# Kernel optimization log

Measured on AMD Instinct MI355X. Metric: run time of the kernel, lower is better.

Reference implementation:

```python
import jax, jax.numpy as jnp
import numpy as np

B = 2
NCLS = 19    # semantic classes for the logits heads
NLAB = 20    # raw point label values 0..19 (0 = unlabeled)
# (Z, Y, X) grids at strides 2, 4, 8 of sizes=[256,256,32]
GRIDS = {2: (16, 128, 128), 4: (8, 64, 64), 8: (4, 32, 32)}


def _lin_idx(coord, Z, Y, X):
    # coord: (N,4) int rows [b, z, y, x] -> flat cell index over B*Z*Y*X
    b, z, y, x = coord[:, 0], coord[:, 1], coord[:, 2], coord[:, 3]
    return ((b * Z + z) * Y + y) * X + x


def _bev_projection(feat, coord, Y, X):
    # Fused equivalent of torch.unique + scatter_max + spconv dense():
    # scatter_max features directly into the dense (B, Y, X) BEV grid keyed by (b,y,x).
    key = (coord[:, 0] * Y + coord[:, 2]) * X + coord[:, 3]
    C = feat.shape[1]
    dense = jax.ops.segment_max(feat, key, num_segments=B * Y * X)  # empty cells -> -inf
    dense = jnp.where(jnp.isfinite(dense), dense, jnp.zeros((), feat.dtype))
    return dense.reshape(B, Y, X, C).transpose(0, 3, 1, 2)  # (B, C, Y, X)


def _voxel_sem_target(fcoord, pcoord, plabel, Z, Y, X):
    # Majority-vote semantic label per point voxel, gathered at feature voxel coords.
    ncell = B * Z * Y * X
    pair = _lin_idx(pcoord, Z, Y, X) * NLAB + plabel  # (cell, label) key
    counts = jax.ops.segment_sum(
        jnp.ones(pcoord.shape[0], jnp.int32), pair, num_segments=ncell * NLAB
    ).reshape(ncell, NLAB)
    maj = jnp.argmax(counts, axis=1).astype(jnp.int32)   # most frequent label per cell
    occ = counts.sum(axis=1) > 0                          # cell contains any point
    fk = _lin_idx(fcoord, Z, Y, X)
    return jnp.where(occ[fk], maj[fk], 0).astype(jnp.int32)  # unmatched -> 0


def _head(x, w1, g, b, w2, b2):
    # Linear(no bias) -> BatchNorm1d(train stats) -> LeakyReLU(0.1) -> Linear
    h = x @ w1
    mu = h.mean(axis=0)
    var = h.var(axis=0)
    h = (h - mu) * jax.lax.rsqrt(var + 1e-5) * g + b
    h = jnp.where(h >= 0, h, 0.1 * h)
    return h @ w2 + b2


def _rand_coords(key, n, Z, Y, X):
    kb, kz, ky, kx = jax.random.split(key, 4)
    return jnp.stack([
        jax.random.randint(kb, (n,), 0, B, dtype=jnp.int32),
        jax.random.randint(kz, (n,), 0, Z, dtype=jnp.int32),
        jax.random.randint(ky, (n,), 0, Y, dtype=jnp.int32),
        jax.random.randint(kx, (n,), 0, X, dtype=jnp.int32),
    ], axis=1)


def setup_inputs() -> dict:
    key = jax.random.key(0)
    ks = jax.random.split(key, 32)
    M1, M2, M3, NP = 200000, 100000, 50000, 500000
    inp = {
        'proj1_vw': jax.random.normal(ks[0], (M1, 64), jnp.float32),
        'proj2_vw': jax.random.normal(ks[1], (M2, 128), jnp.float32),
        'proj3_vw': jax.random.normal(ks[2], (M3, 256), jnp.float32),
        'vw1_coord': _rand_coords(ks[3], M1, *GRIDS[2]),
        'vw2_coord': _rand_coords(ks[4], M2, *GRIDS[4]),
        'vw3_coord': _rand_coords(ks[5], M3, *GRIDS[8]),
        'idx02': _rand_coords(ks[6], NP, *GRIDS[2]),
        'idx04': _rand_coords(ks[7], NP, *GRIDS[4]),
        'idx08': _rand_coords(ks[8], NP, *GRIDS[8]),
        'pw_label': jax.random.randint(ks[9], (NP,), 0, NLAB, dtype=jnp.int32),
    }
    # learned head parameters (out2 / out4 / out8)
    def head_params(k, cin):
        k1, k2 = jax.random.split(k)
        return (jax.random.normal(k1, (cin, 64), jnp.float32) * 0.02,
                jnp.ones((64,), jnp.float32), jnp.zeros((64,), jnp.float32),
                jax.random.normal(k2, (64, NCLS), jnp.float32) * 0.02,
                jnp.zeros((NCLS,), jnp.float32))
    for tag, k, cin in (('h2', ks[10], 64), ('h4', ks[11], 128), ('h8', ks[12], 256)):
        w1, g, b, w2, b2 = head_params(k, cin)
        inp[f'{tag}_w1'], inp[f'{tag}_g'], inp[f'{tag}_b'] = w1, g, b
        inp[f'{tag}_w2'], inp[f'{tag}_b2'] = w2, b2
    return inp


def reference(proj1_vw, proj2_vw, proj3_vw, vw1_coord, vw2_coord, vw3_coord,
              idx02, idx04, idx08, pw_label,
              h2_w1, h2_g, h2_b, h2_w2, h2_b2,
              h4_w1, h4_g, h4_b, h4_w2, h4_b2,
              h8_w1, h8_g, h8_b, h8_w2, h8_b2):
    (Z2, Y2, X2), (Z4, Y4, X4), (Z8, Y8, X8) = GRIDS[2], GRIDS[4], GRIDS[8]
    bev1 = _bev_projection(proj1_vw, vw1_coord, Y2, X2)   # (B, 64, 128, 128)
    bev2 = _bev_projection(proj2_vw, vw2_coord, Y4, X4)   # (B, 128, 64, 64)
    bev3 = _bev_projection(proj3_vw, vw3_coord, Y8, X8)   # (B, 256, 32, 32)
    lbl2 = _voxel_sem_target(vw1_coord, idx02, pw_label, Z2, Y2, X2)
    lbl4 = _voxel_sem_target(vw2_coord, idx04, pw_label, Z4, Y4, X4)
    lbl8 = _voxel_sem_target(vw3_coord, idx08, pw_label, Z8, Y8, X8)
    log2 = _head(proj1_vw, h2_w1, h2_g, h2_b, h2_w2, h2_b2)
    log4 = _head(proj2_vw, h4_w1, h4_g, h4_b, h4_w2, h4_b2)
    log8 = _head(proj3_vw, h8_w1, h8_g, h8_b, h8_w2, h8_b2)
    return (bev1, bev2, bev3, log2, log4, log8, lbl2, lbl4, lbl8)
```

## Files before the change

### kernel.cpp

```cpp
#include <hip/hip_runtime.h>
#include <hip/hip_bf16.h>

typedef unsigned int u32;
typedef unsigned short u16;
typedef __attribute__((ext_vector_type(8))) short short8;
typedef __attribute__((ext_vector_type(4))) float f32x4;

#define NLAB 20

#define M_1 200000
#define C_1 64
#define Z_1 16
#define Y_1 128
#define X_1 128

#define M_2 100000
#define C_2 128
#define Z_2 8
#define Y_2 64
#define X_2 64

#define M_3 50000
#define C_3 256
#define Z_3 4
#define Y_3 32
#define X_3 32

#define O_BEV1 0
#define O_BEV2 2097152
#define O_BEV3 3145728
#define O_LOG1 3670016
#define O_LOG2 7470016
#define O_LOG3 9370016
#define O_LBL1 10320016
#define O_LBL2 10520016
#define O_LBL3 10620016

#define WB_CNT 0
#define WB_CUR 43008
#define WB_PIDX 86016
#define NCELLS 43008
#define SB1 0
#define SB2 32768
#define SB3 40960

#define WBEV_F  4194304
#define WBEV2_F 6291456
#define WBEV3_F 7340032

#define WC1_W 8388608
#define WC2_W 11010048
#define WC3_W 11337728
#define W_COUNT_BYTES 11960320ull
#define WH1 0
#define WH2 12800000
#define WH3 19200000
#define WPART 12000000
#define WP1 0
#define WP2 200064
#define WP3 300160
#define WSTATS 12350208

#define GB1 1563
#define GB2 782
#define GB3 391
#define HB1 782
#define HB2 391
#define HB3 196

static __device__ __forceinline__ u16 f2bf(float f) {
  u32 u = __float_as_uint(f);
  u32 r = u + 0x7fffu + ((u >> 16) & 1u);
  return (u16)(r >> 16);
}

__global__ __launch_bounds__(256) void k_cc(
    const int* __restrict__ co1, const int* __restrict__ co2, const int* __restrict__ co3,
    int* __restrict__ cnt,
    const int* __restrict__ i2, const int* __restrict__ i4, const int* __restrict__ i8,
    const int* __restrict__ lab, u32* __restrict__ hist)
{
  int blk = blockIdx.x;
  if (blk < HB1 + HB2 + HB3) {
    const int* co; int Y, X, M, base, m;
    if (blk < HB1)            { co = co1; Y = Y_1; X = X_1; M = M_1; base = SB1; m = blk * 256 + threadIdx.x; }
    else if (blk < HB1 + HB2) { co = co2; Y = Y_2; X = X_2; M = M_2; base = SB2; m = (blk - HB1) * 256 + threadIdx.x; }
    else                      { co = co3; Y = Y_3; X = X_3; M = M_3; base = SB3; m = (blk - HB1 - HB2) * 256 + threadIdx.x; }
    if (m >= M) return;
    int4 c = *(const int4*)(co + m * 4);
    atomicAdd(cnt + base + (c.x * Y + c.z) * X + c.w, 1);
  } else {
    int cb = blk - (HB1 + HB2 + HB3);
    const int* pc; int Z, Y, X; u32* base; int i;
    if (cb < 1954)      { pc = i2; Z = Z_1; Y = Y_1; X = X_1; base = hist + WC1_W; i = cb * 256 + threadIdx.x; }
    else if (cb < 3908) { pc = i4; Z = Z_2; Y = Y_2; X = X_2; base = hist + WC2_W; i = (cb - 1954) * 256 + threadIdx.x; }
    else                { pc = i8; Z = Z_3; Y = Y_3; X = X_3; base = hist + WC3_W; i = (cb - 3908) * 256 + threadIdx.x; }
    if (i >= 500000) return;
    int4 c = *(const int4*)(pc + i * 4);
    int l = lab[i];
    int lin = ((c.x * Z + c.y) * Y + c.z) * X + c.w;
    atomicAdd(base + lin * 5 + (l >> 2), 1u << ((l & 3) * 8));
  }
}

__global__ __launch_bounds__(1024) void k_scan(const int* __restrict__ cnt, int* __restrict__ cur) {
  int t = threadIdx.x;
  int local[42];
  int s = 0;
#pragma unroll
  for (int j = 0; j < 42; j++) { local[j] = cnt[t * 42 + j]; s += local[j]; }
  __shared__ int red[1024];
  red[t] = s;
  __syncthreads();
  for (int off = 1; off < 1024; off <<= 1) {
    int v = (t >= off) ? red[t - off] : 0;
    __syncthreads();
    red[t] += v;
    __syncthreads();
  }
  int base = red[t] - s;
#pragma unroll
  for (int j = 0; j < 42; j++) { cur[t * 42 + j] = base; base += local[j]; }
}

__global__ __launch_bounds__(256) void k_scatter(
    const int* __restrict__ co1, const int* __restrict__ co2, const int* __restrict__ co3,
    int* __restrict__ cur, int* __restrict__ pidx)
{
  int blk = blockIdx.x;
  const int* co; int Y, X, M, base, m;
  if (blk < HB1)            { co = co1; Y = Y_1; X = X_1; M = M_1; base = SB1; m = blk * 256 + threadIdx.x; }
  else if (blk < HB1 + HB2) { co = co2; Y = Y_2; X = X_2; M = M_2; base = SB2; m = (blk - HB1) * 256 + threadIdx.x; }
  else                      { co = co3; Y = Y_3; X = X_3; M = M_3; base = SB3; m = (blk - HB1 - HB2) * 256 + threadIdx.x; }
  if (m >= M) return;
  int4 c = *(const int4*)(co + m * 4);
  int slot = atomicAdd(cur + base + (c.x * Y + c.z) * X + c.w, 1);
  pidx[slot] = m;
}

#define GBATCH 8
__global__ __launch_bounds__(256) void k_bevgather(
    const float* __restrict__ f1, const float* __restrict__ f2, const float* __restrict__ f3,
    const int* __restrict__ cnt, const int* __restrict__ cur,
    const int* __restrict__ pidx, float* __restrict__ ws)
{
  int w = blockIdx.x * 4 + (threadIdx.x >> 6);
  int lane = threadIdx.x & 63;
  int t0 = w * 4;
  int C = (t0 < 32768) ? 64 : (t0 < 49152) ? 128 : 256;
  const float* fp[4]; int n[4], end_[4]; u32 wb[4];
#pragma unroll
  for (int k = 0; k < 4; k++) {
    int t = t0 + k; const float* f; int cidx; u32 wbv;
    if (t < 32768) {
      f = f1; cidx = SB1 + t; wbv = WBEV_F + (u32)t * 64;
    } else if (t < 49152) {
      int u = t - 32768; int cell = u >> 1, ch = (u & 1) * 64;
      f = f2 + ch; cidx = SB2 + cell; wbv = WBEV2_F + (u32)cell * 128 + ch;
    } else {
      int u = t - 49152; int cell = u >> 2, ch = (u & 3) * 64;
      f = f3 + ch; cidx = SB3 + cell; wbv = WBEV3_F + (u32)cell * 256 + ch;
    }
    fp[k] = f; n[k] = cnt[cidx]; end_[k] = cur[cidx]; wb[k] = wbv;
  }
  int maxn = max(max(n[0], n[1]), max(n[2], n[3]));
  float acc[4];
#pragma unroll
  for (int k = 0; k < 4; k++) acc[k] = __uint_as_float(0xff800000u);
  for (int base = 0; base < maxn; base += GBATCH) {
    int p[4][GBATCH];
#pragma unroll
    for (int k = 0; k < 4; k++) {
      int s = end_[k] - n[k] + base;
      int hi = end_[k] - 1;
#pragma unroll
      for (int j = 0; j < GBATCH; j++) {
        int idx = s + j;
        idx = idx < hi ? idx : hi;
        idx = idx > 0 ? idx : 0;
        p[k][j] = pidx[idx];
      }
    }
    float v[4][GBATCH];
#pragma unroll
    for (int k = 0; k < 4; k++)
#pragma unroll
      for (int j = 0; j < GBATCH; j++)
        v[k][j] = fp[k][(size_t)p[k][j] * C + lane];
#pragma unroll
    for (int k = 0; k < 4; k++)
#pragma unroll
      for (int j = 0; j < GBATCH; j++)
        acc[k] = fmaxf(acc[k], v[k][j]);
  }
#pragma unroll
  for (int k = 0; k < 4; k++)
    ws[wb[k] + lane] = (n[k] > 0) ? acc[k] : 0.f;
}

__global__ __launch_bounds__(256) void k_tl(
    const float* __restrict__ ws, const u32* __restrict__ hist,
    const int* __restrict__ fc1, const int* __restrict__ fc2, const int* __restrict__ fc3,
    float* __restrict__ out)
{
  int blk = blockIdx.x;
  int tid = threadIdx.x;
  if (blk < HB1 + HB2 + HB3) {
    const int* fc; int Z, Y, X, M; const u32* base; long lbase; int m;
    if (blk < HB1)            { fc = fc1; Z = Z_1; Y = Y_1; X = X_1; M = M_1; base = hist + WC1_W; lbase = O_LBL1; m = blk * 256 + tid; }
    else if (blk < HB1 + HB2) { fc = fc2; Z = Z_2; Y = Y_2; X = X_2; M = M_2; base = hist + WC2_W; lbase = O_LBL2; m = (blk - HB1) * 256 + tid; }
    else                      { fc = fc3; Z = Z_3; Y = Y_3; X = X_3; M = M_3; base = hist + WC3_W; lbase = O_LBL3; m = (blk - HB1 - HB2) * 256 + tid; }
    if (m >= M) return;
    int4 c = *(const int4*)(fc + m * 4);
    int lin = ((c.x * Z + c.y) * Y + c.z) * X + c.w;
    const u32* cp = base + lin * 5;
    u32 w0 = cp[0], w1 = cp[1], w2 = cp[2], w3 = cp[3], w4 = cp[4];
    int best = (int)(w0 & 0xffu); int bi = 0;
#pragma unroll
    for (int n = 1; n < NLAB; n++) {
      u32 w = (n < 4) ? w0 : (n < 8) ? w1 : (n < 12) ? w2 : (n < 16) ? w3 : w4;
      int cc = (int)((w >> ((n & 3) * 8)) & 0xffu);
      if (cc > best) { best = cc; bi = n; }
    }
    out[lbase + m] = (float)bi;
    return;
  }
  __shared__ float tileU[4160];
  int bid = blk - (HB1 + HB2 + HB3);
  if (bid < 512) {
    int b = bid >> 8, y = (bid >> 1) & 127, x0 = (bid & 1) * 64;
    const float* src = ws + WBEV_F + (size_t)((b * 128 + y) * 128 + x0) * 64;
#pragma unroll
    for (int pass = 0; pass < 16; pass++) {
      int idx = pass * 256 + tid;
      int x = idx >> 6, c = idx & 63;
      tileU[x * 65 + c] = src[(size_t)x * 64 + c];
    }
    __syncthreads();
    size_t ob = O_BEV1 + ((size_t)(b * 64) * 128 + y) * 128 + x0;
#pragma unroll
    for (int pass = 0; pass < 16; pass++) {
      int idx = pass * 256 + tid;
      int c = idx >> 6, x = idx & 63;
      out[ob + (size_t)c * 16384 + x] = tileU[x * 65 + c];
    }
  } else if (bid < 768) {
    int t = bid - 512;
    int b = t >> 7, y = (t >> 1) & 63, x0 = (t & 1) * 32;
    const float* src = ws + WBEV2_F + (size_t)((b * 64 + y) * 64 + x0) * 128;
#pragma unroll
    for (int pass = 0; pass < 16; pass++) {
      int idx = pass * 256 + tid;
      int x = idx >> 7, c = idx & 127;
      tileU[x * 129 + c] = src[(size_t)x * 128 + c];
    }
    __syncthreads();
    size_t ob = O_BEV2 + ((size_t)(b * 128) * 64 + y) * 64 + x0;
#pragma unroll
    for (int pass = 0; pass < 16; pass++) {
      int idx = pass * 256 + tid;
      int c = idx >> 5, x = idx & 31;
      out[ob + (size_t)c * 4096 + x] = tileU[x * 129 + c];
    }
  } else {
    int t = bid - 768;
    int b = t >> 6, y = (t >> 1) & 31, ch0 = (t & 1) * 128;
    const float* src = ws + WBEV3_F + (size_t)((b * 32 + y) * 32) * 256 + ch0;
#pragma unroll
    for (int pass = 0; pass < 16; pass++) {
      int idx = pass * 256 + tid;
      int x = idx >> 7, c = idx & 127;
      tileU[x * 129 + c] = src[(size_t)x * 256 + c];
    }
    __syncthreads();
    size_t ob = O_BEV3 + ((size_t)(b * 256 + ch0) * 32 + y) * 32;
#pragma unroll
    for (int pass = 0; pass < 16; pass++) {
      int idx = pass * 256 + tid;
      int c = idx >> 5, x = idx & 31;
      out[ob + (size_t)c * 1024 + x] = tileU[x * 129 + c];
    }
  }
}

__global__ __launch_bounds__(256) void k_gemm(
    const float* __restrict__ x1, const float* __restrict__ x2, const float* __restrict__ x3,
    const float* __restrict__ w1a, const float* __restrict__ w1b, const float* __restrict__ w1c,
    u16* __restrict__ hbuf, float* __restrict__ part)
{
  int blk = blockIdx.x;
  const float* x; const float* w1; u16* h; float* pp; int Cin, M, bl, NB;
  if (blk < GB1)            { x = x1; w1 = w1a; h = hbuf + WH1; pp = part + WP1; Cin = C_1; M = M_1; bl = blk;             NB = GB1; }
  else if (blk < GB1 + GB2) { x = x2; w1 = w1b; h = hbuf + WH2; pp = part + WP2; Cin = C_2; M = M_2; bl = blk - GB1;       NB = GB2; }
  else                      { x = x3; w1 = w1c; h = hbuf + WH3; pp = part + WP3; Cin = C_3; M = M_3; bl = blk - GB1 - GB2; NB = GB3; }
  int tid = threadIdx.x;
  int lane = tid & 63, wv = tid >> 6;
  int m16 = lane & 15, quad = lane >> 4;

  __shared__ u16 As[128 * 72];
  __shared__ u16 Bs[64 * 72];
  __shared__ float redS[4][64];
  __shared__ float redQ[4][64];

  f32x4 acc[2][4];
#pragma unroll
  for (int mt = 0; mt < 2; mt++)
#pragma unroll
    for (int nt = 0; nt < 4; nt++) acc[mt][nt] = (f32x4){0.f, 0.f, 0.f, 0.f};

  int nchunk = Cin >> 6;
  for (int c = 0; c < nchunk; c++) {
    if (c) __syncthreads();
#pragma unroll
    for (int pass = 0; pass < 8; pass++) {
      int fidx = pass * 256 + tid;
      int row = fidx >> 4, kp = (fidx & 15) * 4;
      int grow = bl * 128 + row;
      float4 v = make_float4(0.f, 0.f, 0.f, 0.f);
      if (grow < M) v = *(const float4*)(x + (size_t)grow * Cin + c * 64 + kp);
      ushort4 o = { f2bf(v.x), f2bf(v.y), f2bf(v.z), f2bf(v.w) };
      *(ushort4*)(As + row * 72 + kp) = o;
    }
    {
      int n = tid & 63, kg = tid >> 6;
#pragma unroll
      for (int p = 0; p < 4; p++) {
        int k0 = kg * 4 + p * 16;
        const float* wp = w1 + (size_t)(c * 64 + k0) * 64 + n;
        ushort4 o = { f2bf(wp[0]), f2bf(wp[64]), f2bf(wp[128]), f2bf(wp[192]) };
        *(ushort4*)(Bs + n * 72 + k0) = o;
      }
    }
    __syncthreads();
#pragma unroll
    for (int ks = 0; ks < 2; ks++) {
      short8 a0 = *(const short8*)(As + (wv * 32 + m16) * 72 + ks * 32 + quad * 8);
      short8 a1 = *(const short8*)(As + (wv * 32 + 16 + m16) * 72 + ks * 32 + quad * 8);
      short8 b[4];
#pragma unroll
      for (int nt = 0; nt < 4; nt++)
        b[nt] = *(const short8*)(Bs + (nt * 16 + m16) * 72 + ks * 32 + quad * 8);
#pragma unroll
      for (int nt = 0; nt < 4; nt++) {
        acc[0][nt] = __builtin_amdgcn_mfma_f32_16x16x32_bf16(a0, b[nt], acc[0][nt], 0, 0, 0);
        acc[1][nt] = __builtin_amdgcn_mfma_f32_16x16x32_bf16(a1, b[nt], acc[1][nt], 0, 0, 0);
      }
    }
  }

  float s[4] = {0.f, 0.f, 0.f, 0.f}, q[4] = {0.f, 0.f, 0.f, 0.f};
#pragma unroll
  for (int mt = 0; mt < 2; mt++) {
#pragma unroll
    for (int nt = 0; nt < 4; nt++) {
#pragma unroll
      for (int r = 0; r < 4; r++) {
        float v = acc[mt][nt][r];
        int grow = bl * 128 + wv * 32 + mt * 16 + quad * 4 + r;
        if (grow < M) h[(size_t)grow * 64 + nt * 16 + m16] = f2bf(v);
        s[nt] += v;
        q[nt] = fmaf(v, v, q[nt]);
      }
    }
  }
#pragma unroll
  for (int nt = 0; nt < 4; nt++) {
    s[nt] += __shfl_xor(s[nt], 16); s[nt] += __shfl_xor(s[nt], 32);
    q[nt] += __shfl_xor(q[nt], 16); q[nt] += __shfl_xor(q[nt], 32);
  }
  if (lane < 16) {
#pragma unroll
    for (int nt = 0; nt < 4; nt++) {
      redS[wv][nt * 16 + lane] = s[nt];
      redQ[wv][nt * 16 + lane] = q[nt];
    }
  }
  __syncthreads();
  if (tid < 64) {
    pp[tid * NB + bl] = redS[0][tid] + redS[1][tid] + redS[2][tid] + redS[3][tid];
  } else if (tid < 128) {
    int n2 = tid - 64;
    pp[(64 + n2) * NB + bl] = redQ[0][n2] + redQ[1][n2] + redQ[2][n2] + redQ[3][n2];
  }
}

__global__ __launch_bounds__(256) void k_stats(const float* __restrict__ part, float* __restrict__ stats,
    const float* __restrict__ g1, const float* __restrict__ b1,
    const float* __restrict__ g4, const float* __restrict__ b4,
    const float* __restrict__ g8, const float* __restrict__ b8)
{
  int blk = blockIdx.x;
  int sc = blk >> 6, col = blk & 63;
  int nb; const float* p; float invM; const float* g; const float* bb;
  if (sc == 0)      { nb = GB1; p = part + WP1; invM = 1.f / M_1; g = g1; bb = b1; }
  else if (sc == 1) { nb = GB2; p = part + WP2; invM = 1.f / M_2; g = g4; bb = b4; }
  else              { nb = GB3; p = part + WP3; invM = 1.f / M_3; g = g8; bb = b8; }
  int t = threadIdx.x;
  const float* ps = p + (size_t)col * nb;
  const float* pq = p + (size_t)(64 + col) * nb;
  float s = 0.f, q = 0.f;
  for (int i = t; i < nb; i += 256) { s += ps[i]; q += pq[i]; }
  __shared__ float r1[256], r2[256];
  r1[t] = s; r2[t] = q;
  __syncthreads();
  for (int off = 128; off > 0; off >>= 1) {
    if (t < off) { r1[t] += r1[t + off]; r2[t] += r2[t + off]; }
    __syncthreads();
  }
  if (t == 0) {
    float mu  = r1[0] * invM;
    float var = r2[0] * invM - mu * mu;
    float scale = rsqrtf(var + 1e-5f) * g[col];
    stats[sc * 128 + col]      = scale;
    stats[sc * 128 + 64 + col] = fmaf(-mu, scale, bb[col]);
  }
}

__global__ __launch_bounds__(256) void k_head(
    const u16* __restrict__ hbuf, const float* __restrict__ stats,
    const float* __restrict__ w21, const float* __restrict__ c21,
    const float* __restrict__ w24, const float* __restrict__ c24,
    const float* __restrict__ w28, const float* __restrict__ c28,
    float* __restrict__ out)
{
  int blk = blockIdx.x;
  const u16* h; const float* st; const float* w2; const float* b2;
  int M; long obase; int bl;
  if (blk < HB1)            { h = hbuf + WH1; st = stats;       w2 = w21; b2 = c21; M = M_1; obase = O_LOG1; bl = blk; }
  else if (blk < HB1 + HB2) { h = hbuf + WH2; st = stats + 128; w2 = w24; b2 = c24; M = M_2; obase = O_LOG2; bl = blk - HB1; }
  else                      { h = hbuf + WH3; st = stats + 256; w2 = w28; b2 = c28; M = M_3; obase = O_LOG3; bl = blk - HB1 - HB2; }
  int tid = threadIdx.x;
  int rowbase = bl * 256;
  int avail = M - rowbase; if (avail > 256) avail = 256;

  __shared__ __align__(16) float os[256 * 19];

  float acc[19];
#pragma unroll
  for (int n = 0; n < 19; n++) acc[n] = 0.f;

  if (tid < avail) {
    const uint4* hr = (const uint4*)(h + (size_t)(rowbase + tid) * 64);
    uint4 d[8];
#pragma unroll
    for (int q = 0; q < 8; q++) d[q] = hr[q];
#pragma unroll
    for (int q = 0; q < 8; q++) {
#pragma unroll
      for (int half = 0; half < 2; half++) {
        u32 dx = half ? d[q].z : d[q].x;
        u32 dy = half ? d[q].w : d[q].y;
        int j = q * 8 + half * 4;
        float f0 = __uint_as_float(dx << 16);
        float f1 = __uint_as_float(dx & 0xffff0000u);
        float f2 = __uint_as_float(dy << 16);
        float f3 = __uint_as_float(dy & 0xffff0000u);
        float a0 = fmaf(f0, st[j],     st[64 + j]);     a0 = a0 >= 0.f ? a0 : 0.1f * a0;
        float a1 = fmaf(f1, st[j + 1], st[64 + j + 1]); a1 = a1 >= 0.f ? a1 : 0.1f * a1;
        float a2 = fmaf(f2, st[j + 2], st[64 + j + 2]); a2 = a2 >= 0.f ? a2 : 0.1f * a2;
        float a3 = fmaf(f3, st[j + 3], st[64 + j + 3]); a3 = a3 >= 0.f ? a3 : 0.1f * a3;
#pragma unroll
        for (int n = 0; n < 19; n++) {
          acc[n] = fmaf(a0, w2[j * 19 + n], acc[n]);
          acc[n] = fmaf(a1, w2[(j + 1) * 19 + n], acc[n]);
          acc[n] = fmaf(a2, w2[(j + 2) * 19 + n], acc[n]);
          acc[n] = fmaf(a3, w2[(j + 3) * 19 + n], acc[n]);
        }
      }
    }
#pragma unroll
    for (int n = 0; n < 19; n++) os[tid * 19 + n] = acc[n] + b2[n];
  }
  __syncthreads();
  int tot = avail * 19;
  float* op = out + obase + (size_t)rowbase * 19;
  for (int i = tid; i < tot; i += 256) op[i] = os[i];
}

extern "C" void kernel_launch(void* const* d_in, const int* in_sizes, int n_in,
                              void* d_out, int out_size, void* d_ws, size_t ws_size,
                              hipStream_t stream) {
  (void)in_sizes; (void)n_in; (void)out_size; (void)ws_size;
  const float* p1 = (const float*)d_in[0];
  const float* p2 = (const float*)d_in[1];
  const float* p3 = (const float*)d_in[2];
  const int* vc1  = (const int*)d_in[3];
  const int* vc2  = (const int*)d_in[4];
  const int* vc3  = (const int*)d_in[5];
  const int* i2   = (const int*)d_in[6];
  const int* i4   = (const int*)d_in[7];
  const int* i8   = (const int*)d_in[8];
  const int* lab  = (const int*)d_in[9];
  const float* h2w1 = (const float*)d_in[10]; const float* h2g = (const float*)d_in[11];
  const float* h2b  = (const float*)d_in[12]; const float* h2w2 = (const float*)d_in[13];
  const float* h2b2 = (const float*)d_in[14];
  const float* h4w1 = (const float*)d_in[15]; const float* h4g = (const float*)d_in[16];
  const float* h4b  = (const float*)d_in[17]; const float* h4w2 = (const float*)d_in[18];
  const float* h4b2 = (const float*)d_in[19];
  const float* h8w1 = (const float*)d_in[20]; const float* h8g = (const float*)d_in[21];
  const float* h8b  = (const float*)d_in[22]; const float* h8w2 = (const float*)d_in[23];
  const float* h8b2 = (const float*)d_in[24];

  float* out = (float*)d_out;
  int* wsi = (int*)d_ws;
  u32* wsu = (u32*)d_ws;
  float* wsf = (float*)d_ws;
  u16* wsh = (u16*)d_ws;

  hipMemsetAsync(wsi + WB_CNT, 0, NCELLS * sizeof(int), stream);
  hipMemsetAsync(wsu + WC1_W, 0, W_COUNT_BYTES, stream);

  k_cc<<<HB1 + HB2 + HB3 + 5862, 256, 0, stream>>>(vc1, vc2, vc3, wsi + WB_CNT,
      i2, i4, i8, lab, wsu);
  k_scan<<<1, 1024, 0, stream>>>(wsi + WB_CNT, wsi + WB_CUR);
  k_scatter<<<HB1 + HB2 + HB3, 256, 0, stream>>>(vc1, vc2, vc3, wsi + WB_CUR, wsi + WB_PIDX);

  k_bevgather<<<3584, 256, 0, stream>>>(p1, p2, p3,
      wsi + WB_CNT, wsi + WB_CUR, wsi + WB_PIDX, wsf);

  k_tl<<<HB1 + HB2 + HB3 + 896, 256, 0, stream>>>(wsf, wsu, vc1, vc2, vc3, out);

  k_gemm<<<GB1 + GB2 + GB3, 256, 0, stream>>>(p1, p2, p3, h2w1, h4w1, h8w1, wsh, wsf + WPART);
  k_stats<<<192, 256, 0, stream>>>(wsf + WPART, wsf + WSTATS, h2g, h2b, h4g, h4b, h8g, h8b);
  k_head<<<HB1 + HB2 + HB3, 256, 0, stream>>>((const u16*)d_ws, wsf + WSTATS,
      h2w2, h2b2, h4w2, h4b2, h8w2, h8b2, out);
}
```

Before: 464.2 us.

## Fuse GEMM, BEV gather and label histogram into one mega-kernel launch

When the workspace is large enough, the pipeline is rescheduled. Only the cell count runs first, then one kernel runs the head GEMM, the BEV gather and the label histogram together. The BN stats reduction is folded into the label/transpose kernel, and the GEMM outputs move to non-overlapping workspace regions so they can run alongside the gather. This removes launches and lets independent, differently bounded work share the GPU, at the cost of more workspace and a larger heterogeneous grid. A fallback keeps the old sequence when the workspace is small.

```diff
diff --git a/kernel.cpp b/kernel.cpp
--- a/kernel.cpp
+++ b/kernel.cpp
@@ -52,14 +52,20 @@
 #define WC2_W 11010048
 #define WC3_W 11337728
 #define W_COUNT_BYTES 11960320ull
+
 #define WH1 0
 #define WH2 12800000
 #define WH3 19200000
-#define WPART 12000000
 #define WP1 0
 #define WP2 200064
 #define WP3 300160
-#define WSTATS 12350208
+
+#define WPART_SMALL 12000000
+#define WSTATS_SMALL 12350208
+#define WH_BIG_U16  22806528
+#define WPART_BIG   22603264
+#define WSTATS_BIG  22953472
+#define WS_BIG_NEED 92000000ull
 
 #define GB1 1563
 #define GB2 782
@@ -74,78 +80,40 @@
   return (u16)(r >> 16);
 }
 
-__global__ __launch_bounds__(256) void k_cc(
-    const int* __restrict__ co1, const int* __restrict__ co2, const int* __restrict__ co3,
-    int* __restrict__ cnt,
-    const int* __restrict__ i2, const int* __restrict__ i4, const int* __restrict__ i8,
-    const int* __restrict__ lab, u32* __restrict__ hist)
-{
-  int blk = blockIdx.x;
-  if (blk < HB1 + HB2 + HB3) {
-    const int* co; int Y, X, M, base, m;
-    if (blk < HB1)            { co = co1; Y = Y_1; X = X_1; M = M_1; base = SB1; m = blk * 256 + threadIdx.x; }
-    else if (blk < HB1 + HB2) { co = co2; Y = Y_2; X = X_2; M = M_2; base = SB2; m = (blk - HB1) * 256 + threadIdx.x; }
-    else                      { co = co3; Y = Y_3; X = X_3; M = M_3; base = SB3; m = (blk - HB1 - HB2) * 256 + threadIdx.x; }
-    if (m >= M) return;
-    int4 c = *(const int4*)(co + m * 4);
-    atomicAdd(cnt + base + (c.x * Y + c.z) * X + c.w, 1);
-  } else {
-    int cb = blk - (HB1 + HB2 + HB3);
-    const int* pc; int Z, Y, X; u32* base; int i;
-    if (cb < 1954)      { pc = i2; Z = Z_1; Y = Y_1; X = X_1; base = hist + WC1_W; i = cb * 256 + threadIdx.x; }
-    else if (cb < 3908) { pc = i4; Z = Z_2; Y = Y_2; X = X_2; base = hist + WC2_W; i = (cb - 1954) * 256 + threadIdx.x; }
-    else                { pc = i8; Z = Z_3; Y = Y_3; X = X_3; base = hist + WC3_W; i = (cb - 3908) * 256 + threadIdx.x; }
-    if (i >= 500000) return;
-    int4 c = *(const int4*)(pc + i * 4);
-    int l = lab[i];
-    int lin = ((c.x * Z + c.y) * Y + c.z) * X + c.w;
-    atomicAdd(base + lin * 5 + (l >> 2), 1u << ((l & 3) * 8));
-  }
-}
-
-__global__ __launch_bounds__(1024) void k_scan(const int* __restrict__ cnt, int* __restrict__ cur) {
-  int t = threadIdx.x;
-  int local[42];
-  int s = 0;
-#pragma unroll
-  for (int j = 0; j < 42; j++) { local[j] = cnt[t * 42 + j]; s += local[j]; }
-  __shared__ int red[1024];
-  red[t] = s;
-  __syncthreads();
-  for (int off = 1; off < 1024; off <<= 1) {
-    int v = (t >= off) ? red[t - off] : 0;
-    __syncthreads();
-    red[t] += v;
-    __syncthreads();
-  }
-  int base = red[t] - s;
-#pragma unroll
-  for (int j = 0; j < 42; j++) { cur[t * 42 + j] = base; base += local[j]; }
-}
-
-__global__ __launch_bounds__(256) void k_scatter(
-    const int* __restrict__ co1, const int* __restrict__ co2, const int* __restrict__ co3,
-    int* __restrict__ cur, int* __restrict__ pidx)
-{
-  int blk = blockIdx.x;
+
+static __device__ __forceinline__ void dev_cellcount(int blk, int tid,
+    const int* co1, const int* co2, const int* co3, int* cnt)
+{
   const int* co; int Y, X, M, base, m;
-  if (blk < HB1)            { co = co1; Y = Y_1; X = X_1; M = M_1; base = SB1; m = blk * 256 + threadIdx.x; }
-  else if (blk < HB1 + HB2) { co = co2; Y = Y_2; X = X_2; M = M_2; base = SB2; m = (blk - HB1) * 256 + threadIdx.x; }
-  else                      { co = co3; Y = Y_3; X = X_3; M = M_3; base = SB3; m = (blk - HB1 - HB2) * 256 + threadIdx.x; }
+  if (blk < HB1)            { co = co1; Y = Y_1; X = X_1; M = M_1; base = SB1; m = blk * 256 + tid; }
+  else if (blk < HB1 + HB2) { co = co2; Y = Y_2; X = X_2; M = M_2; base = SB2; m = (blk - HB1) * 256 + tid; }
+  else                      { co = co3; Y = Y_3; X = X_3; M = M_3; base = SB3; m = (blk - HB1 - HB2) * 256 + tid; }
   if (m >= M) return;
   int4 c = *(const int4*)(co + m * 4);
-  int slot = atomicAdd(cur + base + (c.x * Y + c.z) * X + c.w, 1);
-  pidx[slot] = m;
+  atomicAdd(cnt + base + (c.x * Y + c.z) * X + c.w, 1);
+}
+
+static __device__ __forceinline__ void dev_count(int cb, int tid,
+    const int* i2, const int* i4, const int* i8, const int* lab, u32* hist)
+{
+  const int* pc; int Z, Y, X; u32* base; int i;
+  if (cb < 1954)      { pc = i2; Z = Z_1; Y = Y_1; X = X_1; base = hist + WC1_W; i = cb * 256 + tid; }
+  else if (cb < 3908) { pc = i4; Z = Z_2; Y = Y_2; X = X_2; base = hist + WC2_W; i = (cb - 1954) * 256 + tid; }
+  else                { pc = i8; Z = Z_3; Y = Y_3; X = X_3; base = hist + WC3_W; i = (cb - 3908) * 256 + tid; }
+  if (i >= 500000) return;
+  int4 c = *(const int4*)(pc + i * 4);
+  int l = lab[i];
+  int lin = ((c.x * Z + c.y) * Y + c.z) * X + c.w;
+  atomicAdd(base + lin * 5 + (l >> 2), 1u << ((l & 3) * 8));
 }
 
 #define GBATCH 8
-__global__ __launch_bounds__(256) void k_bevgather(
-    const float* __restrict__ f1, const float* __restrict__ f2, const float* __restrict__ f3,
-    const int* __restrict__ cnt, const int* __restrict__ cur,
-    const int* __restrict__ pidx, float* __restrict__ ws)
-{
-  int w = blockIdx.x * 4 + (threadIdx.x >> 6);
-  int lane = threadIdx.x & 63;
+static __device__ __forceinline__ void dev_gather(int gb, int tid,
+    const float* f1, const float* f2, const float* f3,
+    const int* cnt, const int* cur, const int* pidx, float* ws)
+{
+  int w = gb * 4 + (tid >> 6);
+  int lane = tid & 63;
   int t0 = w * 4;
   int C = (t0 < 32768) ? 64 : (t0 < 49152) ? 128 : 256;
   const float* fp[4]; int n[4], end_[4]; u32 wb[4];
@@ -198,102 +166,15 @@
     ws[wb[k] + lane] = (n[k] > 0) ? acc[k] : 0.f;
 }
 
-__global__ __launch_bounds__(256) void k_tl(
-    const float* __restrict__ ws, const u32* __restrict__ hist,
-    const int* __restrict__ fc1, const int* __restrict__ fc2, const int* __restrict__ fc3,
-    float* __restrict__ out)
-{
-  int blk = blockIdx.x;
-  int tid = threadIdx.x;
-  if (blk < HB1 + HB2 + HB3) {
-    const int* fc; int Z, Y, X, M; const u32* base; long lbase; int m;
-    if (blk < HB1)            { fc = fc1; Z = Z_1; Y = Y_1; X = X_1; M = M_1; base = hist + WC1_W; lbase = O_LBL1; m = blk * 256 + tid; }
-    else if (blk < HB1 + HB2) { fc = fc2; Z = Z_2; Y = Y_2; X = X_2; M = M_2; base = hist + WC2_W; lbase = O_LBL2; m = (blk - HB1) * 256 + tid; }
-    else                      { fc = fc3; Z = Z_3; Y = Y_3; X = X_3; M = M_3; base = hist + WC3_W; lbase = O_LBL3; m = (blk - HB1 - HB2) * 256 + tid; }
-    if (m >= M) return;
-    int4 c = *(const int4*)(fc + m * 4);
-    int lin = ((c.x * Z + c.y) * Y + c.z) * X + c.w;
-    const u32* cp = base + lin * 5;
-    u32 w0 = cp[0], w1 = cp[1], w2 = cp[2], w3 = cp[3], w4 = cp[4];
-    int best = (int)(w0 & 0xffu); int bi = 0;
-#pragma unroll
-    for (int n = 1; n < NLAB; n++) {
-      u32 w = (n < 4) ? w0 : (n < 8) ? w1 : (n < 12) ? w2 : (n < 16) ? w3 : w4;
-      int cc = (int)((w >> ((n & 3) * 8)) & 0xffu);
-      if (cc > best) { best = cc; bi = n; }
-    }
-    out[lbase + m] = (float)bi;
-    return;
-  }
-  __shared__ float tileU[4160];
-  int bid = blk - (HB1 + HB2 + HB3);
-  if (bid < 512) {
-    int b = bid >> 8, y = (bid >> 1) & 127, x0 = (bid & 1) * 64;
-    const float* src = ws + WBEV_F + (size_t)((b * 128 + y) * 128 + x0) * 64;
-#pragma unroll
-    for (int pass = 0; pass < 16; pass++) {
-      int idx = pass * 256 + tid;
-      int x = idx >> 6, c = idx & 63;
-      tileU[x * 65 + c] = src[(size_t)x * 64 + c];
-    }
-    __syncthreads();
-    size_t ob = O_BEV1 + ((size_t)(b * 64) * 128 + y) * 128 + x0;
-#pragma unroll
-    for (int pass = 0; pass < 16; pass++) {
-      int idx = pass * 256 + tid;
-      int c = idx >> 6, x = idx & 63;
-      out[ob + (size_t)c * 16384 + x] = tileU[x * 65 + c];
-    }
-  } else if (bid < 768) {
-    int t = bid - 512;
-    int b = t >> 7, y = (t >> 1) & 63, x0 = (t & 1) * 32;
-    const float* src = ws + WBEV2_F + (size_t)((b * 64 + y) * 64 + x0) * 128;
-#pragma unroll
-    for (int pass = 0; pass < 16; pass++) {
-      int idx = pass * 256 + tid;
-      int x = idx >> 7, c = idx & 127;
-      tileU[x * 129 + c] = src[(size_t)x * 128 + c];
-    }
-    __syncthreads();
-    size_t ob = O_BEV2 + ((size_t)(b * 128) * 64 + y) * 64 + x0;
-#pragma unroll
-    for (int pass = 0; pass < 16; pass++) {
-      int idx = pass * 256 + tid;
-      int c = idx >> 5, x = idx & 31;
-      out[ob + (size_t)c * 4096 + x] = tileU[x * 129 + c];
-    }
-  } else {
-    int t = bid - 768;
-    int b = t >> 6, y = (t >> 1) & 31, ch0 = (t & 1) * 128;
-    const float* src = ws + WBEV3_F + (size_t)((b * 32 + y) * 32) * 256 + ch0;
-#pragma unroll
-    for (int pass = 0; pass < 16; pass++) {
-      int idx = pass * 256 + tid;
-      int x = idx >> 7, c = idx & 127;
-      tileU[x * 129 + c] = src[(size_t)x * 256 + c];
-    }
-    __syncthreads();
-    size_t ob = O_BEV3 + ((size_t)(b * 256 + ch0) * 32 + y) * 32;
-#pragma unroll
-    for (int pass = 0; pass < 16; pass++) {
-      int idx = pass * 256 + tid;
-      int c = idx >> 5, x = idx & 31;
-      out[ob + (size_t)c * 1024 + x] = tileU[x * 129 + c];
-    }
-  }
-}
-
-__global__ __launch_bounds__(256) void k_gemm(
-    const float* __restrict__ x1, const float* __restrict__ x2, const float* __restrict__ x3,
-    const float* __restrict__ w1a, const float* __restrict__ w1b, const float* __restrict__ w1c,
-    u16* __restrict__ hbuf, float* __restrict__ part)
-{
-  int blk = blockIdx.x;
+static __device__ __forceinline__ void dev_gemm(int blk, int tid,
+    const float* x1, const float* x2, const float* x3,
+    const float* w1a, const float* w1b, const float* w1c,
+    u16* hbuf, float* part)
+{
   const float* x; const float* w1; u16* h; float* pp; int Cin, M, bl, NB;
   if (blk < GB1)            { x = x1; w1 = w1a; h = hbuf + WH1; pp = part + WP1; Cin = C_1; M = M_1; bl = blk;             NB = GB1; }
   else if (blk < GB1 + GB2) { x = x2; w1 = w1b; h = hbuf + WH2; pp = part + WP2; Cin = C_2; M = M_2; bl = blk - GB1;       NB = GB2; }
   else                      { x = x3; w1 = w1c; h = hbuf + WH3; pp = part + WP3; Cin = C_3; M = M_3; bl = blk - GB1 - GB2; NB = GB3; }
-  int tid = threadIdx.x;
   int lane = tid & 63, wv = tid >> 6;
   int m16 = lane & 15, quad = lane >> 4;
 
@@ -384,35 +265,231 @@
   }
 }
 
-__global__ __launch_bounds__(256) void k_stats(const float* __restrict__ part, float* __restrict__ stats,
-    const float* __restrict__ g1, const float* __restrict__ b1,
-    const float* __restrict__ g4, const float* __restrict__ b4,
-    const float* __restrict__ g8, const float* __restrict__ b8)
-{
-  int blk = blockIdx.x;
-  int sc = blk >> 6, col = blk & 63;
+static __device__ __forceinline__ void dev_lbl(int blk, int tid,
+    const int* fc1, const int* fc2, const int* fc3, const u32* hist, float* out)
+{
+  const int* fc; int Z, Y, X, M; const u32* base; long lbase; int m;
+  if (blk < HB1)            { fc = fc1; Z = Z_1; Y = Y_1; X = X_1; M = M_1; base = hist + WC1_W; lbase = O_LBL1; m = blk * 256 + tid; }
+  else if (blk < HB1 + HB2) { fc = fc2; Z = Z_2; Y = Y_2; X = X_2; M = M_2; base = hist + WC2_W; lbase = O_LBL2; m = (blk - HB1) * 256 + tid; }
+  else                      { fc = fc3; Z = Z_3; Y = Y_3; X = X_3; M = M_3; base = hist + WC3_W; lbase = O_LBL3; m = (blk - HB1 - HB2) * 256 + tid; }
+  if (m >= M) return;
+  int4 c = *(const int4*)(fc + m * 4);
+  int lin = ((c.x * Z + c.y) * Y + c.z) * X + c.w;
+  const u32* cp = base + lin * 5;
+  u32 w0 = cp[0], w1 = cp[1], w2 = cp[2], w3 = cp[3], w4 = cp[4];
+  int best = (int)(w0 & 0xffu); int bi = 0;
+#pragma unroll
+  for (int n = 1; n < NLAB; n++) {
+    u32 w = (n < 4) ? w0 : (n < 8) ? w1 : (n < 12) ? w2 : (n < 16) ? w3 : w4;
+    int cc = (int)((w >> ((n & 3) * 8)) & 0xffu);
+    if (cc > best) { best = cc; bi = n; }
+  }
+  out[lbase + m] = (float)bi;
+}
+
+static __device__ __forceinline__ void dev_transpose(int bid, int tid,
+    const float* ws, float* out)
+{
+  __shared__ float tileU[4160];
+  if (bid < 512) {
+    int b = bid >> 8, y = (bid >> 1) & 127, x0 = (bid & 1) * 64;
+    const float* src = ws + WBEV_F + (size_t)((b * 128 + y) * 128 + x0) * 64;
+#pragma unroll
+    for (int pass = 0; pass < 16; pass++) {
+      int idx = pass * 256 + tid;
+      int x = idx >> 6, c = idx & 63;
+      tileU[x * 65 + c] = src[(size_t)x * 64 + c];
+    }
+    __syncthreads();
+    size_t ob = O_BEV1 + ((size_t)(b * 64) * 128 + y) * 128 + x0;
+#pragma unroll
+    for (int pass = 0; pass < 16; pass++) {
+      int idx = pass * 256 + tid;
+      int c = idx >> 6, x = idx & 63;
+      out[ob + (size_t)c * 16384 + x] = tileU[x * 65 + c];
+    }
+  } else if (bid < 768) {
+    int t = bid - 512;
+    int b = t >> 7, y = (t >> 1) & 63, x0 = (t & 1) * 32;
+    const float* src = ws + WBEV2_F + (size_t)((b * 64 + y) * 64 + x0) * 128;
+#pragma unroll
+    for (int pass = 0; pass < 16; pass++) {
+      int idx = pass * 256 + tid;
+      int x = idx >> 7, c = idx & 127;
+      tileU[x * 129 + c] = src[(size_t)x * 128 + c];
+    }
+    __syncthreads();
+    size_t ob = O_BEV2 + ((size_t)(b * 128) * 64 + y) * 64 + x0;
+#pragma unroll
+    for (int pass = 0; pass < 16; pass++) {
+      int idx = pass * 256 + tid;
+      int c = idx >> 5, x = idx & 31;
+      out[ob + (size_t)c * 4096 + x] = tileU[x * 129 + c];
+    }
+  } else {
+    int t = bid - 768;
+    int b = t >> 6, y = (t >> 1) & 31, ch0 = (t & 1) * 128;
+    const float* src = ws + WBEV3_F + (size_t)((b * 32 + y) * 32) * 256 + ch0;
+#pragma unroll
+    for (int pass = 0; pass < 16; pass++) {
+      int idx = pass * 256 + tid;
+      int x = idx >> 7, c = idx & 127;
+      tileU[x * 129 + c] = src[(size_t)x * 256 + c];
+    }
+    __syncthreads();
+    size_t ob = O_BEV3 + ((size_t)(b * 256 + ch0) * 32 + y) * 32;
+#pragma unroll
+    for (int pass = 0; pass < 16; pass++) {
+      int idx = pass * 256 + tid;
+      int c = idx >> 5, x = idx & 31;
+      out[ob + (size_t)c * 1024 + x] = tileU[x * 129 + c];
+    }
+  }
+}
+
+static __device__ __forceinline__ void dev_stats(int sblk, int tid,
+    const float* part, float* stats,
+    const float* g1, const float* b1, const float* g4, const float* b4,
+    const float* g8, const float* b8)
+{
+  int sc = sblk >> 6, col = sblk & 63;
   int nb; const float* p; float invM; const float* g; const float* bb;
   if (sc == 0)      { nb = GB1; p = part + WP1; invM = 1.f / M_1; g = g1; bb = b1; }
   else if (sc == 1) { nb = GB2; p = part + WP2; invM = 1.f / M_2; g = g4; bb = b4; }
   else              { nb = GB3; p = part + WP3; invM = 1.f / M_3; g = g8; bb = b8; }
-  int t = threadIdx.x;
   const float* ps = p + (size_t)col * nb;
   const float* pq = p + (size_t)(64 + col) * nb;
   float s = 0.f, q = 0.f;
-  for (int i = t; i < nb; i += 256) { s += ps[i]; q += pq[i]; }
+  for (int i = tid; i < nb; i += 256) { s += ps[i]; q += pq[i]; }
   __shared__ float r1[256], r2[256];
-  r1[t] = s; r2[t] = q;
+  r1[tid] = s; r2[tid] = q;
   __syncthreads();
   for (int off = 128; off > 0; off >>= 1) {
-    if (t < off) { r1[t] += r1[t + off]; r2[t] += r2[t + off]; }
+    if (tid < off) { r1[tid] += r1[tid + off]; r2[tid] += r2[tid + off]; }
     __syncthreads();
   }
-  if (t == 0) {
+  if (tid == 0) {
     float mu  = r1[0] * invM;
     float var = r2[0] * invM - mu * mu;
     float scale = rsqrtf(var + 1e-5f) * g[col];
     stats[sc * 128 + col]      = scale;
     stats[sc * 128 + 64 + col] = fmaf(-mu, scale, bb[col]);
+  }
+}
+
+
+__global__ __launch_bounds__(256) void k_pre(
+    const int* __restrict__ co1, const int* __restrict__ co2, const int* __restrict__ co3,
+    int* __restrict__ cnt)
+{
+  dev_cellcount(blockIdx.x, threadIdx.x, co1, co2, co3, cnt);
+}
+
+__global__ __launch_bounds__(256) void k_cc(
+    const int* __restrict__ co1, const int* __restrict__ co2, const int* __restrict__ co3,
+    int* __restrict__ cnt,
+    const int* __restrict__ i2, const int* __restrict__ i4, const int* __restrict__ i8,
+    const int* __restrict__ lab, u32* __restrict__ hist)
+{
+  int blk = blockIdx.x;
+  if (blk < HB1 + HB2 + HB3) dev_cellcount(blk, threadIdx.x, co1, co2, co3, cnt);
+  else dev_count(blk - (HB1 + HB2 + HB3), threadIdx.x, i2, i4, i8, lab, hist);
+}
+
+__global__ __launch_bounds__(1024) void k_scan(const int* __restrict__ cnt, int* __restrict__ cur) {
+  int t = threadIdx.x;
+  int local[42];
+  int s = 0;
+#pragma unroll
+  for (int j = 0; j < 42; j++) { local[j] = cnt[t * 42 + j]; s += local[j]; }
+  __shared__ int red[1024];
+  red[t] = s;
+  __syncthreads();
+  for (int off = 1; off < 1024; off <<= 1) {
+    int v = (t >= off) ? red[t - off] : 0;
+    __syncthreads();
+    red[t] += v;
+    __syncthreads();
+  }
+  int base = red[t] - s;
+#pragma unroll
+  for (int j = 0; j < 42; j++) { cur[t * 42 + j] = base; base += local[j]; }
+}
+
+__global__ __launch_bounds__(256) void k_scatter(
+    const int* __restrict__ co1, const int* __restrict__ co2, const int* __restrict__ co3,
+    int* __restrict__ cur, int* __restrict__ pidx)
+{
+  int blk = blockIdx.x;
+  const int* co; int Y, X, M, base, m;
+  if (blk < HB1)            { co = co1; Y = Y_1; X = X_1; M = M_1; base = SB1; m = blk * 256 + threadIdx.x; }
+  else if (blk < HB1 + HB2) { co = co2; Y = Y_2; X = X_2; M = M_2; base = SB2; m = (blk - HB1) * 256 + threadIdx.x; }
+  else                      { co = co3; Y = Y_3; X = X_3; M = M_3; base = SB3; m = (blk - HB1 - HB2) * 256 + threadIdx.x; }
+  if (m >= M) return;
+  int4 c = *(const int4*)(co + m * 4);
+  int slot = atomicAdd(cur + base + (c.x * Y + c.z) * X + c.w, 1);
+  pidx[slot] = m;
+}
+
+__global__ __launch_bounds__(256) void k_mega(
+    const float* __restrict__ x1, const float* __restrict__ x2, const float* __restrict__ x3,
+    const float* __restrict__ w1a, const float* __restrict__ w1b, const float* __restrict__ w1c,
+    u16* __restrict__ hbuf, float* __restrict__ part,
+    const int* __restrict__ cnt, const int* __restrict__ cur, const int* __restrict__ pidx,
+    float* __restrict__ ws,
+    const int* __restrict__ i2, const int* __restrict__ i4, const int* __restrict__ i8,
+    const int* __restrict__ lab, u32* __restrict__ hist)
+{
+  int blk = blockIdx.x;
+  if (blk < GB1 + GB2 + GB3) {
+    dev_gemm(blk, threadIdx.x, x1, x2, x3, w1a, w1b, w1c, hbuf, part);
+  } else if (blk < GB1 + GB2 + GB3 + 3584) {
+    dev_gather(blk - (GB1 + GB2 + GB3), threadIdx.x, x1, x2, x3, cnt, cur, pidx, ws);
+  } else {
+    dev_count(blk - (GB1 + GB2 + GB3 + 3584), threadIdx.x, i2, i4, i8, lab, hist);
+  }
+}
+
+__global__ __launch_bounds__(256) void k_bevgather(
+    const float* __restrict__ f1, const float* __restrict__ f2, const float* __restrict__ f3,
+    const int* __restrict__ cnt, const int* __restrict__ cur,
+    const int* __restrict__ pidx, float* __restrict__ ws)
+{
+  dev_gather(blockIdx.x, threadIdx.x, f1, f2, f3, cnt, cur, pidx, ws);
+}
+
+__global__ __launch_bounds__(256) void k_gemm(
+    const float* __restrict__ x1, const float* __restrict__ x2, const float* __restrict__ x3,
+    const float* __restrict__ w1a, const float* __restrict__ w1b, const float* __restrict__ w1c,
+    u16* __restrict__ hbuf, float* __restrict__ part)
+{
+  dev_gemm(blockIdx.x, threadIdx.x, x1, x2, x3, w1a, w1b, w1c, hbuf, part);
+}
+
+__global__ __launch_bounds__(256) void k_stats(const float* __restrict__ part, float* __restrict__ stats,
+    const float* __restrict__ g1, const float* __restrict__ b1,
+    const float* __restrict__ g4, const float* __restrict__ b4,
+    const float* __restrict__ g8, const float* __restrict__ b8)
+{
+  dev_stats(blockIdx.x, threadIdx.x, part, stats, g1, b1, g4, b4, g8, b8);
+}
+
+__global__ __launch_bounds__(256) void k_tl(
+    const float* __restrict__ ws, const u32* __restrict__ hist,
+    const int* __restrict__ fc1, const int* __restrict__ fc2, const int* __restrict__ fc3,
+    float* __restrict__ out,
+    const float* __restrict__ part, float* __restrict__ stats,
+    const float* __restrict__ g1, const float* __restrict__ b1,
+    const float* __restrict__ g4, const float* __restrict__ b4,
+    const float* __restrict__ g8, const float* __restrict__ b8)
+{
+  int blk = blockIdx.x;
+  if (blk < HB1 + HB2 + HB3) {
+    dev_lbl(blk, threadIdx.x, fc1, fc2, fc3, hist, out);
+  } else if (blk < HB1 + HB2 + HB3 + 896) {
+    dev_transpose(blk - (HB1 + HB2 + HB3), threadIdx.x, ws, out);
+  } else {
+    dev_stats(blk - (HB1 + HB2 + HB3 + 896), threadIdx.x, part, stats, g1, b1, g4, b4, g8, b8);
   }
 }
 
@@ -480,7 +557,7 @@
 extern "C" void kernel_launch(void* const* d_in, const int* in_sizes, int n_in,
                               void* d_out, int out_size, void* d_ws, size_t ws_size,
                               hipStream_t stream) {
-  (void)in_sizes; (void)n_in; (void)out_size; (void)ws_size;
+  (void)in_sizes; (void)n_in; (void)out_size;
   const float* p1 = (const float*)d_in[0];
   const float* p2 = (const float*)d_in[1];
   const float* p3 = (const float*)d_in[2];
@@ -510,18 +587,33 @@
   hipMemsetAsync(wsi + WB_CNT, 0, NCELLS * sizeof(int), stream);
   hipMemsetAsync(wsu + WC1_W, 0, W_COUNT_BYTES, stream);
 
-  k_cc<<<HB1 + HB2 + HB3 + 5862, 256, 0, stream>>>(vc1, vc2, vc3, wsi + WB_CNT,
-      i2, i4, i8, lab, wsu);
-  k_scan<<<1, 1024, 0, stream>>>(wsi + WB_CNT, wsi + WB_CUR);
-  k_scatter<<<HB1 + HB2 + HB3, 256, 0, stream>>>(vc1, vc2, vc3, wsi + WB_CUR, wsi + WB_PIDX);
-
-  k_bevgather<<<3584, 256, 0, stream>>>(p1, p2, p3,
-      wsi + WB_CNT, wsi + WB_CUR, wsi + WB_PIDX, wsf);
-
-  k_tl<<<HB1 + HB2 + HB3 + 896, 256, 0, stream>>>(wsf, wsu, vc1, vc2, vc3, out);
-
-  k_gemm<<<GB1 + GB2 + GB3, 256, 0, stream>>>(p1, p2, p3, h2w1, h4w1, h8w1, wsh, wsf + WPART);
-  k_stats<<<192, 256, 0, stream>>>(wsf + WPART, wsf + WSTATS, h2g, h2b, h4g, h4b, h8g, h8b);
-  k_head<<<HB1 + HB2 + HB3, 256, 0, stream>>>((const u16*)d_ws, wsf + WSTATS,
-      h2w2, h2b2, h4w2, h4b2, h8w2, h8b2, out);
-}
+  if (ws_size >= WS_BIG_NEED) {
+    u16* hbig = wsh + WH_BIG_U16;
+    float* pbig = wsf + WPART_BIG;
+    float* sbig = wsf + WSTATS_BIG;
+    k_pre<<<HB1 + HB2 + HB3, 256, 0, stream>>>(vc1, vc2, vc3, wsi + WB_CNT);
+    k_scan<<<1, 1024, 0, stream>>>(wsi + WB_CNT, wsi + WB_CUR);
+    k_scatter<<<HB1 + HB2 + HB3, 256, 0, stream>>>(vc1, vc2, vc3, wsi + WB_CUR, wsi + WB_PIDX);
+    k_mega<<<GB1 + GB2 + GB3 + 3584 + 5862, 256, 0, stream>>>(p1, p2, p3,
+        h2w1, h4w1, h8w1, hbig, pbig,
+        wsi + WB_CNT, wsi + WB_CUR, wsi + WB_PIDX, wsf,
+        i2, i4, i8, lab, wsu);
+    k_tl<<<HB1 + HB2 + HB3 + 896 + 192, 256, 0, stream>>>(wsf, wsu, vc1, vc2, vc3, out,
+        pbig, sbig, h2g, h2b, h4g, h4b, h8g, h8b);
+    k_head<<<HB1 + HB2 + HB3, 256, 0, stream>>>(hbig, sbig,
+        h2w2, h2b2, h4w2, h4b2, h8w2, h8b2, out);
+  } else {
+    k_cc<<<HB1 + HB2 + HB3 + 5862, 256, 0, stream>>>(vc1, vc2, vc3, wsi + WB_CNT,
+        i2, i4, i8, lab, wsu);
+    k_scan<<<1, 1024, 0, stream>>>(wsi + WB_CNT, wsi + WB_CUR);
+    k_scatter<<<HB1 + HB2 + HB3, 256, 0, stream>>>(vc1, vc2, vc3, wsi + WB_CUR, wsi + WB_PIDX);
+    k_bevgather<<<3584, 256, 0, stream>>>(p1, p2, p3,
+        wsi + WB_CNT, wsi + WB_CUR, wsi + WB_PIDX, wsf);
+    k_tl<<<HB1 + HB2 + HB3 + 896, 256, 0, stream>>>(wsf, wsu, vc1, vc2, vc3, out,
+        (const float*)d_ws, wsf, h2g, h2b, h4g, h4b, h8g, h8b);
+    k_gemm<<<GB1 + GB2 + GB3, 256, 0, stream>>>(p1, p2, p3, h2w1, h4w1, h8w1, wsh, wsf + WPART_SMALL);
+    k_stats<<<192, 256, 0, stream>>>(wsf + WPART_SMALL, wsf + WSTATS_SMALL, h2g, h2b, h4g, h4b, h8g, h8b);
+    k_head<<<HB1 + HB2 + HB3, 256, 0, stream>>>((const u16*)d_ws, wsf + WSTATS_SMALL,
+        h2w2, h2b2, h4w2, h4b2, h8w2, h8b2, out);
+  }
+}
```

New measurement: 440.4 us. 1.05x faster.
